# Optimization experiments

Measured on AMD Instinct MI355X. Metric: run time of the kernel, lower is better.

## Reference

```python
import jax, jax.numpy as jnp
import numpy as np

H = 2; C = 64          # heads, hidden_channels
N = 50000; E = 800000  # nodes, edges
D = 128                # input_dim
EPS = 1e-5

def _lrelu(x, s):
    return jnp.where(x >= 0, x, s * x)

def _ln(x, g, b):
    m = x.mean(-1, keepdims=True)
    v = ((x - m) ** 2).mean(-1, keepdims=True)
    return (x - m) / jnp.sqrt(v + EPS) * g + b

def _gatv2(x_src, x_dst, src, dst, Wl, bl, Wr, br, att, Wres, bias):
    # PyG GATv2Conv: concat=False (mean over heads), residual=True, no self loops
    n = x_dst.shape[0]
    xl = (x_src @ Wl + bl).reshape(-1, H, C)  # [Ns,H,C]
    xr = (x_dst @ Wr + br).reshape(-1, H, C)  # [Nd,H,C]
    xj = xl[src]                               # [E,H,C] messages from source
    xi = xr[dst]                               # [E,H,C]
    e = _lrelu(xi + xj, 0.2)
    alpha = jnp.einsum('ehc,hc->eh', e, att)   # [E,H]
    amax = jax.lax.stop_gradient(jax.ops.segment_max(alpha, dst, num_segments=n))
    ex = jnp.exp(alpha - amax[dst])
    den = jax.ops.segment_sum(ex, dst, num_segments=n)
    a = ex / den[dst]                          # segment softmax over incoming edges
    out = jax.ops.segment_sum(xj * a[:, :, None], dst, num_segments=n)  # [Nd,H,C]
    return out.mean(axis=1) + x_dst @ Wres + bias


def setup_inputs() -> dict:
    key = jax.random.key(0)
    ks = jax.random.split(key, 40)
    d = {}
    d['x'] = jax.random.normal(ks[0], (N, D), jnp.float32)
    d['edge_index'] = jax.random.randint(ks[1], (2, E), 0, N, jnp.int32)
    i = 2
    for p, ind in (('c1d', D), ('c1t', D), ('c2d', C), ('c2t', C)):
        d[p + '_Wl'] = jax.random.normal(ks[i], (ind, H * C), jnp.float32) * 0.05; i += 1
        d[p + '_bl'] = jnp.zeros((H * C,), jnp.float32)
        d[p + '_Wr'] = jax.random.normal(ks[i], (ind, H * C), jnp.float32) * 0.05; i += 1
        d[p + '_br'] = jnp.zeros((H * C,), jnp.float32)
        d[p + '_att'] = jax.random.normal(ks[i], (H, C), jnp.float32) * 0.05; i += 1
        d[p + '_Wres'] = jax.random.normal(ks[i], (ind, C), jnp.float32) * 0.05; i += 1
        d[p + '_bias'] = jnp.zeros((C,), jnp.float32)
    d['nd_g'] = jnp.ones((C,), jnp.float32); d['nd_b'] = jnp.zeros((C,), jnp.float32)
    d['nt_g'] = jnp.ones((C,), jnp.float32); d['nt_b'] = jnp.zeros((C,), jnp.float32)
    return d


def reference(x, edge_index, c1d_Wl, c1d_bl, c1d_Wr, c1d_br, c1d_att, c1d_Wres, c1d_bias, c1t_Wl, c1t_bl, c1t_Wr, c1t_br, c1t_att, c1t_Wres, c1t_bias, c2d_Wl, c2d_bl, c2d_Wr, c2d_br, c2d_att, c2d_Wres, c2d_bias, c2t_Wl, c2t_bl, c2t_Wr, c2t_br, c2t_att, c2t_Wres, c2t_bias, nd_g, nd_b, nt_g, nt_b):
    src, dst = edge_index[0], edge_index[1]
    dep = _gatv2(x, x, src, dst, c1d_Wl, c1d_bl, c1d_Wr, c1d_br, c1d_att, c1d_Wres, c1d_bias)
    dep = _lrelu(_ln(dep, nd_g, nd_b), 0.01)
    dant = _gatv2(x, x, dst, src, c1t_Wl, c1t_bl, c1t_Wr, c1t_br, c1t_att, c1t_Wres, c1t_bias)
    dant = _lrelu(_ln(dant, nt_g, nt_b), 0.01)
    dep2 = _lrelu(_gatv2(dep, dep, src, dst, c2d_Wl, c2d_bl, c2d_Wr, c2d_br, c2d_att, c2d_Wres, c2d_bias), 0.01)
    dant2 = _lrelu(_gatv2(dant, dant, dst, src, c2t_Wl, c2t_bl, c2t_Wr, c2t_br, c2t_att, c2t_Wres, c2t_bias), 0.01)
    return jnp.concatenate([dep2, dant2, x], axis=-1)
```

## Files before the change

kernel.cpp:

```cpp
#include <hip/hip_runtime.h>
#include <math.h>

typedef unsigned short ushort_t;
typedef __attribute__((ext_vector_type(8))) short short8x;
typedef __attribute__((ext_vector_type(4))) float f32x4;

#define CSHIFT 9
#define CC 12288
#define EPB 4096
#define ECAP 1024
#define NCMAX 128

__device__ __forceinline__ unsigned f2bf(float f) {
  unsigned u = __float_as_uint(f);
  u += 0x7fff + ((u >> 16) & 1);
  return u >> 16;
}
__device__ __forceinline__ float bf2f(ushort_t u) {
  return __uint_as_float(((unsigned)u) << 16);
}
__device__ __forceinline__ float dpp_red8(float v) {
  v += __int_as_float(__builtin_amdgcn_update_dpp(0, __float_as_int(v), 0xB1, 0xF, 0xF, true));
  v += __int_as_float(__builtin_amdgcn_update_dpp(0, __float_as_int(v), 0x4E, 0xF, 0xF, true));
  v += __int_as_float(__builtin_amdgcn_update_dpp(0, __float_as_int(v), 0x141, 0xF, 0xF, true));
  return v;
}

struct GArgs {
  const float* Wl[2];
  const float* bl[2];
  const float* Wr[2];
  const float* br[2];
  const float* Wres[2];
  const float* bias[2];
};

__device__ __forceinline__ float wval1(const GArgs& ga, int col, int k) {
  int dir = col >= 320 ? 1 : 0;
  int cc = col - dir * 320;
  return cc < 128 ? ga.Wl[dir][k * 128 + cc]
       : cc < 256 ? ga.Wr[dir][k * 128 + (cc - 128)]
                  : ga.Wres[dir][k * 64 + (cc - 256)];
}
__device__ __forceinline__ float bval(const GArgs& ga, int col) {
  int dir = col >= 320 ? 1 : 0;
  int cc = col - dir * 320;
  return cc < 128 ? ga.bl[dir][cc]
       : cc < 256 ? ga.br[dir][cc - 128]
                  : ga.bias[dir][cc - 256];
}


__global__ __launch_bounds__(128) void pack_kernel(GArgs g1, GArgs g2,
                                                   ushort_t* __restrict__ WT1,
                                                   ushort_t* __restrict__ WT2,
                                                   float* __restrict__ bc1,
                                                   float* __restrict__ bc2) {
  int b = blockIdx.x;
  int k = threadIdx.x;
  if (b < 640) {
    WT1[b * 128 + k] = (ushort_t)f2bf(wval1(g1, b, k));
  } else if (b < 1280) {
    int c = b - 640;
    int dir = c >= 320 ? 1 : 0;
    int cc = c - dir * 320;
    float v = 0.f;
    if ((k >> 6) == dir) {
      int k2 = k & 63;
      v = cc < 128 ? g2.Wl[dir][k2 * 128 + cc]
        : cc < 256 ? g2.Wr[dir][k2 * 128 + (cc - 128)]
                   : g2.Wres[dir][k2 * 64 + (cc - 256)];
    }
    WT2[c * 128 + k] = (ushort_t)f2bf(v);
  } else {
    for (int c = k; c < 640; c += 128) {
      bc1[c] = bval(g1, c);
      bc2[c] = bval(g2, c);
    }
  }
}


template <int AF32>
__device__ __forceinline__ void gemm_body(const float* Af, const ushort_t* Ab,
                                          const ushort_t* WT, const float* bc,
                                          ushort_t* Y, int N, int rb, int cb,
                                          ushort_t* lds) {
  const int tid = threadIdx.x;
  const int lane = tid & 63;
  const int w = tid >> 6;
  const int m0 = rb * 64;
  const int cbase = cb * 128 + w * 32;

#pragma unroll
  for (int c = 0; c < 4; ++c) {
    int Lb = (tid + c * 256) * 16;
    int row = Lb >> 8, within = Lb & 255;
    int so = within ^ ((row & 7) << 4);
    int grow = m0 + row;
    if (grow >= N) grow = N - 1;
    if (AF32) {
      const float* src = Af + (size_t)grow * 128 + (so >> 1);
      float4 a = *(const float4*)src;
      float4 b = *(const float4*)(src + 4);
      uint4 o;
      o.x = f2bf(a.x) | (f2bf(a.y) << 16);
      o.y = f2bf(a.z) | (f2bf(a.w) << 16);
      o.z = f2bf(b.x) | (f2bf(b.y) << 16);
      o.w = f2bf(b.z) | (f2bf(b.w) << 16);
      ((uint4*)lds)[tid + c * 256] = o;
    } else {
      ((uint4*)lds)[tid + c * 256] = *(const uint4*)(Ab + (size_t)grow * 128 + (so >> 1));
    }
  }

  short8x bf[4][2];
#pragma unroll
  for (int ks = 0; ks < 4; ++ks)
#pragma unroll
    for (int ns = 0; ns < 2; ++ns) {
      int col = cbase + ns * 16 + (lane & 15);
      bf[ks][ns] = *(const short8x*)(WT + (size_t)col * 128 + ks * 32 + (lane >> 4) * 8);
    }

  __syncthreads();

  f32x4 z = {0.f, 0.f, 0.f, 0.f};
  f32x4 acc[4][2];
#pragma unroll
  for (int ms = 0; ms < 4; ++ms) {
    acc[ms][0] = z;
    acc[ms][1] = z;
  }
#pragma unroll
  for (int ks = 0; ks < 4; ++ks) {
    short8x af[4];
#pragma unroll
    for (int ms = 0; ms < 4; ++ms) {
      int row = ms * 16 + (lane & 15);
      int byte = row * 256 + ((ks * 64 + (lane >> 4) * 16) ^ ((row & 7) << 4));
      af[ms] = *(const short8x*)((const char*)lds + byte);
    }
#pragma unroll
    for (int ms = 0; ms < 4; ++ms) {
      acc[ms][0] = __builtin_amdgcn_mfma_f32_16x16x32_bf16(af[ms], bf[ks][0], acc[ms][0], 0, 0, 0);
      acc[ms][1] = __builtin_amdgcn_mfma_f32_16x16x32_bf16(af[ms], bf[ks][1], acc[ms][1], 0, 0, 0);
    }
  }

#pragma unroll
  for (int ms = 0; ms < 4; ++ms)
#pragma unroll
    for (int ns = 0; ns < 2; ++ns) {
      int col = cbase + ns * 16 + (lane & 15);
      float bv = bc[col];
#pragma unroll
      for (int r = 0; r < 4; ++r) {
        int grow = m0 + ms * 16 + (lane >> 4) * 4 + r;
        if (grow < N) Y[(size_t)grow * 640 + col] = (ushort_t)f2bf(acc[ms][ns][r] + bv);
      }
    }
}


__global__ __launch_bounds__(256) void k_front(
    const float* __restrict__ x, const int* __restrict__ ei, int E, int N,
    int* __restrict__ gc0, int* __restrict__ gc1, int* __restrict__ ctail0,
    int* __restrict__ ctail1, const ushort_t* __restrict__ WT1,
    const float* __restrict__ bc1, ushort_t* __restrict__ Y,
    float* __restrict__ out, int nbinA, int ngemm, int nrow) {
  __shared__ ushort_t lds[8192];
  const int bid = blockIdx.x;
  const int t = threadIdx.x;
  if (bid < nbinA) {
    int* h0 = (int*)lds;
    int* h1 = h0 + NCMAX;
    int* b0 = h1 + NCMAX;
    int* b1 = b0 + NCMAX;
    const int e0 = bid * EPB;
    const int e1 = min(e0 + EPB, E);
    for (int i = t; i < NCMAX; i += 256) {
      h0[i] = 0;
      h1[i] = 0;
    }
    __syncthreads();
    for (int i = e0 + t; i < e1; i += 256) {
      int s = ei[i], d = ei[E + i];
      atomicAdd(&h0[d >> CSHIFT], 1);
      atomicAdd(&h1[s >> CSHIFT], 1);
    }
    __syncthreads();
    for (int c = t; c < NCMAX; c += 256) {
      int n0 = h0[c], n1 = h1[c];
      b0[c] = n0 ? atomicAdd(&ctail0[c], n0) : 0;
      b1[c] = n1 ? atomicAdd(&ctail1[c], n1) : 0;
      h0[c] = 0;
      h1[c] = 0;
    }
    __syncthreads();
    for (int i = e0 + t; i < e1; i += 256) {
      int s = ei[i], d = ei[E + i];
      int c0 = d >> CSHIFT;
      int p0 = b0[c0] + atomicAdd(&h0[c0], 1);
      if (p0 < CC) gc0[c0 * CC + p0] = (s << 16) | d;
      int c1 = s >> CSHIFT;
      int p1 = b1[c1] + atomicAdd(&h1[c1], 1);
      if (p1 < CC) gc1[c1 * CC + p1] = (d << 16) | s;
    }
  } else if (bid < nbinA + ngemm) {
    int gb = bid - nbinA;
    gemm_body<1>(x, nullptr, WT1, bc1, Y, N, gb % nrow, gb / nrow, lds);
  } else {
    int i = (bid - nbinA - ngemm) * 256 + t;
    if (i < N * 32) {
      float4 v = ((const float4*)x)[i];
      ((float4*)out)[(size_t)(i >> 5) * 64 + 32 + (i & 31)] = v;
    }
  }
}


__global__ __launch_bounds__(256) void gemm2_kernel(const ushort_t* __restrict__ A,
                                                    const ushort_t* __restrict__ WT,
                                                    const float* __restrict__ bc,
                                                    ushort_t* __restrict__ Y, int N) {
  __shared__ ushort_t lds[8192];
  gemm_body<0>(nullptr, A, WT, bc, Y, N, blockIdx.x, blockIdx.y, lds);
}


template <int MODE>
__global__ __launch_bounds__(256) void agg_bucket(
    const ushort_t* __restrict__ Y, const int* __restrict__ gc0,
    const int* __restrict__ gc1, const int* __restrict__ ctail0,
    const int* __restrict__ ctail1, const float* __restrict__ attA,
    const float* __restrict__ attB, const float* __restrict__ lng0,
    const float* __restrict__ lnb0, const float* __restrict__ lng1,
    const float* __restrict__ lnb1, void* __restrict__ outp, int N) {
  __shared__ int ebuf[ECAP];
  __shared__ int lnbr[ECAP + 8];
  __shared__ int hist[32], offs[32], cur[32];
  __shared__ int ecnt;
  const int fb = blockIdx.x;
  const int cb = fb >> 4;
  const int dir = blockIdx.y;
  const int t = threadIdx.x;
  const int* gc = dir ? gc1 : gc0;
  const int* ctail = dir ? ctail1 : ctail0;
  const float* att = dir ? attB : attA;

  for (int i = t; i < ECAP + 8; i += 256) lnbr[i] = 0;
  if (t < 32) {
    hist[t] = 0;
    cur[t] = 0;
  }
  if (t == 64) ecnt = 0;
  __syncthreads();

  {
    const int cntc = min(ctail[cb], CC);
    const int* src = gc + cb * CC;
    for (int i = t; i < cntc; i += 256) {
      int e = src[i];
      if (((e & 0xFFFF) >> 5) == fb) {
        int idx = atomicAdd(&ecnt, 1);
        if (idx < ECAP) ebuf[idx] = e;
      }
    }
  }
  __syncthreads();
  const int tot = min(ecnt, ECAP);
  for (int i = t; i < tot; i += 256) atomicAdd(&hist[ebuf[i] & 31], 1);
  __syncthreads();
  if (t < 32) {
    int v = hist[t], inc = v;
#pragma unroll
    for (int o = 1; o < 32; o <<= 1) {
      int u = __shfl_up(inc, o);
      if (t >= o) inc += u;
    }
    offs[t] = inc - v;
  }
  __syncthreads();
  for (int i = t; i < tot; i += 256) {
    int e = ebuf[i];
    int r = e & 31;
    lnbr[offs[r] + atomicAdd(&cur[r], 1)] = (int)((unsigned)e >> 16) * 1280;
  }
  __syncthreads();

  const int wv = t >> 6, lane = t & 63, g = lane >> 4, jj = lane & 15;
  const float L2E = 1.4426950408889634f;
  float av[8];
  {
    float4 a0 = *(const float4*)(att + jj * 8);
    float4 a1 = *(const float4*)(att + jj * 8 + 4);
    av[0] = a0.x * L2E; av[1] = a0.y * L2E; av[2] = a0.z * L2E; av[3] = a0.w * L2E;
    av[4] = a1.x * L2E; av[5] = a1.y * L2E; av[6] = a1.z * L2E; av[7] = a1.w * L2E;
  }
  const char* Yb = (const char*)Y + dir * 640 + jj * 16;

  for (int r = wv; r < 32; r += 4) {
    const int n = fb * 32 + r;
    if (n >= N) break;
    const char* rowp = (const char*)Y + (size_t)n * 1280 + dir * 640;

    float xi[8];
    {
      short8x v = *(const short8x*)(rowp + 256 + jj * 16);
#pragma unroll
      for (int q = 0; q < 8; ++q) xi[q] = bf2f((ushort_t)v[q]);
    }
    float d = 0.f;
    float acc[8];
#pragma unroll
    for (int q = 0; q < 8; ++q) acc[q] = 0.f;

    const int beg = offs[r], deg = hist[r];
    if (deg > 0) {
      int off = lnbr[beg + g];
      short8x vj = *(const short8x*)(Yb + (size_t)(unsigned)off);
      for (int k0 = 0; k0 < deg; k0 += 4) {
        int offn = lnbr[beg + k0 + 4 + g];
        short8x vn = *(const short8x*)(Yb + (size_t)(unsigned)offn);
        float xj[8];
#pragma unroll
        for (int q = 0; q < 8; ++q) xj[q] = bf2f((ushort_t)vj[q]);
        float p = 0.f;
#pragma unroll
        for (int q = 0; q < 8; ++q) {
          float e = xi[q] + xj[q];
          e = fmaxf(e, 0.2f * e);
          p = fmaf(e, av[q], p);
        }
        p = dpp_red8(p);
        float wgt = (k0 + g < deg) ? __builtin_amdgcn_exp2f(p) : 0.f;
        d += wgt;
#pragma unroll
        for (int q = 0; q < 8; ++q) acc[q] = fmaf(xj[q], wgt, acc[q]);
        vj = vn;
      }
#pragma unroll
      for (int o = 16; o <= 32; o <<= 1) {
        d += __shfl_xor(d, o);
#pragma unroll
        for (int q = 0; q < 8; ++q) acc[q] += __shfl_xor(acc[q], o);
      }
    }
    float inv = deg > 0 ? 1.f / d : 0.f;
    float v[8];
#pragma unroll
    for (int q = 0; q < 8; ++q) {
      float tq = acc[q] * inv;
      v[q] = 0.5f * (tq + __shfl_xor(tq, 8));
    }
    {
      short8x rv = *(const short8x*)(rowp + 512 + (jj & 7) * 16);
#pragma unroll
      for (int q = 0; q < 8; ++q) v[q] += bf2f((ushort_t)rv[q]);
    }

    if (MODE == 0) {
      float s = 0.f;
#pragma unroll
      for (int q = 0; q < 8; ++q) s += v[q];
      s += __shfl_xor(s, 1);
      s += __shfl_xor(s, 2);
      s += __shfl_xor(s, 4);
      float mu = s * (1.f / 64.f);
      float vs = 0.f;
#pragma unroll
      for (int q = 0; q < 8; ++q) {
        float dv = v[q] - mu;
        vs += dv * dv;
      }
      vs += __shfl_xor(vs, 1);
      vs += __shfl_xor(vs, 2);
      vs += __shfl_xor(vs, 4);
      float rstd = rsqrtf(vs * (1.f / 64.f) + 1e-5f);
      if (g == 0 && jj < 8) {
        const float* lg = dir ? lng1 : lng0;
        const float* lb = dir ? lnb1 : lnb0;
        unsigned o2[8];
#pragma unroll
        for (int q = 0; q < 8; ++q) {
          int c = jj * 8 + q;
          float y = (v[q] - mu) * rstd * lg[c] + lb[c];
          y = fmaxf(y, 0.01f * y);
          o2[q] = f2bf(y);
        }
        uint4 pk;
        pk.x = o2[0] | (o2[1] << 16);
        pk.y = o2[2] | (o2[3] << 16);
        pk.z = o2[4] | (o2[5] << 16);
        pk.w = o2[6] | (o2[7] << 16);
        *(uint4*)((ushort_t*)outp + (size_t)n * 128 + dir * 64 + jj * 8) = pk;
      }
    } else {
      if (g == 0 && jj < 8) {
        float* op = (float*)outp + (size_t)n * 256 + dir * 64 + jj * 8;
        float4 o0, o1;
        o0.x = fmaxf(v[0], 0.01f * v[0]);
        o0.y = fmaxf(v[1], 0.01f * v[1]);
        o0.z = fmaxf(v[2], 0.01f * v[2]);
        o0.w = fmaxf(v[3], 0.01f * v[3]);
        o1.x = fmaxf(v[4], 0.01f * v[4]);
        o1.y = fmaxf(v[5], 0.01f * v[5]);
        o1.z = fmaxf(v[6], 0.01f * v[6]);
        o1.w = fmaxf(v[7], 0.01f * v[7]);
        *(float4*)op = o0;
        *(float4*)(op + 4) = o1;
      }
    }
  }
}


extern "C" void kernel_launch(void* const* d_in, const int* in_sizes, int n_in,
                              void* d_out, int out_size, void* d_ws, size_t ws_size,
                              hipStream_t stream) {
  const float* x = (const float*)d_in[0];
  const int* ei = (const int*)d_in[1];
  const int N = in_sizes[0] / 128;
  const int E = in_sizes[1] / 2;
  float* out = (float*)d_out;
  const int nbuck = (N + 31) >> 5;
  const int ncoarse = (N + (1 << CSHIFT) - 1) >> CSHIFT;

  char* p = (char*)d_ws;
  auto carve = [&](size_t bytes) {
    char* q = p;
    p += ((bytes + 255) & ~(size_t)255);
    return q;
  };
  int* ctail = (int*)carve(2 * NCMAX * 4);
  int* gc0 = (int*)carve((size_t)ncoarse * CC * 4);
  int* gc1 = (int*)carve((size_t)ncoarse * CC * 4);
  ushort_t* Y1 = (ushort_t*)carve((size_t)N * 640 * 2);
  ushort_t* A2 = (ushort_t*)carve((size_t)N * 128 * 2);
  ushort_t* WT1 = (ushort_t*)carve(640 * 128 * 2);
  ushort_t* WT2 = (ushort_t*)carve(640 * 128 * 2);
  float* bc1 = (float*)carve(640 * 4);
  float* bc2 = (float*)carve(640 * 4);
  int* ctail0 = ctail;
  int* ctail1 = ctail + NCMAX;

  auto F = [&](int i) { return (const float*)d_in[i]; };
  GArgs g1, g2;
  g1.Wl[0] = F(2);  g1.bl[0] = F(3);  g1.Wr[0] = F(4);  g1.br[0] = F(5);
  g1.Wres[0] = F(7); g1.bias[0] = F(8);
  g1.Wl[1] = F(9);  g1.bl[1] = F(10); g1.Wr[1] = F(11); g1.br[1] = F(12);
  g1.Wres[1] = F(14); g1.bias[1] = F(15);
  g2.Wl[0] = F(16); g2.bl[0] = F(17); g2.Wr[0] = F(18); g2.br[0] = F(19);
  g2.Wres[0] = F(21); g2.bias[0] = F(22);
  g2.Wl[1] = F(23); g2.bl[1] = F(24); g2.Wr[1] = F(25); g2.br[1] = F(26);
  g2.Wres[1] = F(28); g2.bias[1] = F(29);

  hipMemsetAsync(ctail, 0, 2 * NCMAX * 4, stream);

  pack_kernel<<<1281, 128, 0, stream>>>(g1, g2, WT1, WT2, bc1, bc2);

  const int nbinA = (E + EPB - 1) / EPB;
  const int nrow = (N + 63) / 64;
  const int ngemm = nrow * 5;
  const int ncopy = (N * 32 + 255) / 256;
  k_front<<<nbinA + ngemm + ncopy, 256, 0, stream>>>(
      x, ei, E, N, gc0, gc1, ctail0, ctail1, WT1, bc1, Y1, out,
      nbinA, ngemm, nrow);

  const dim3 ga(nbuck, 2);
  agg_bucket<0><<<ga, 256, 0, stream>>>(Y1, gc0, gc1, ctail0, ctail1, F(6), F(13),
                                        F(30), F(31), F(32), F(33), A2, N);
  gemm2_kernel<<<dim3(nrow, 5), 256, 0, stream>>>(A2, WT2, bc2, Y1, N);
  agg_bucket<1><<<ga, 256, 0, stream>>>(Y1, gc0, gc1, ctail0, ctail1, F(20), F(27),
                                        nullptr, nullptr, nullptr, nullptr, out, N);
}
```

Measured before the change: 305.8 us.

## Split LeakyReLU attention into abs term plus precomputed per-source exponential factor

Rewrites LeakyReLU(e) as 0.6e + 0.4|e|. The destination-only linear term cancels in the softmax, and the source-only linear term becomes a per-node factor exp(0.6·att·(W_l x + b_l)), computed by new kmat blocks in the front and second-layer GEMM kernels and stored in bf16. The per-edge inner loop then needs only an fabs-weighted dot product and one multiply by the gathered factor, instead of a max and an extra multiply per channel. In exchange it adds an extra 2-byte gather per edge, new precompute blocks, and some bf16 rounding of the exponential factor.

```diff
diff --git a/kernel.cpp b/kernel.cpp
--- a/kernel.cpp
+++ b/kernel.cpp
@@ -11,6 +11,9 @@
 #define ECAP 1024
 #define NCMAX 128
 
+#define C06L2E 0.8656170245333781f
+#define C04L2E 0.5770780163555854f
+
 __device__ __forceinline__ unsigned f2bf(float f) {
   unsigned u = __float_as_uint(f);
   u += 0x7fff + ((u >> 16) & 1);
@@ -23,6 +26,11 @@
   v += __int_as_float(__builtin_amdgcn_update_dpp(0, __float_as_int(v), 0xB1, 0xF, 0xF, true));
   v += __int_as_float(__builtin_amdgcn_update_dpp(0, __float_as_int(v), 0x4E, 0xF, 0xF, true));
   v += __int_as_float(__builtin_amdgcn_update_dpp(0, __float_as_int(v), 0x141, 0xF, 0xF, true));
+  return v;
+}
+__device__ __forceinline__ float dpp_red16(float v) {
+  v = dpp_red8(v);
+  v += __int_as_float(__builtin_amdgcn_update_dpp(0, __float_as_int(v), 0x140, 0xF, 0xF, true));
   return v;
 }
 
@@ -51,11 +59,13 @@
 }
 
 
-__global__ __launch_bounds__(128) void pack_kernel(GArgs g1, GArgs g2,
-                                                   ushort_t* __restrict__ WT1,
-                                                   ushort_t* __restrict__ WT2,
-                                                   float* __restrict__ bc1,
-                                                   float* __restrict__ bc2) {
+__global__ __launch_bounds__(128) void pack_kernel(
+    GArgs g1, GArgs g2, const float* __restrict__ a1d0,
+    const float* __restrict__ a1d1, const float* __restrict__ a2d0,
+    const float* __restrict__ a2d1, ushort_t* __restrict__ WT1,
+    ushort_t* __restrict__ WT2, float* __restrict__ bc1,
+    float* __restrict__ bc2, float* __restrict__ WS1,
+    float* __restrict__ WS2, float* __restrict__ sb) {
   int b = blockIdx.x;
   int k = threadIdx.x;
   if (b < 640) {
@@ -72,10 +82,37 @@
                    : g2.Wres[dir][k2 * 64 + (cc - 256)];
     }
     WT2[c * 128 + k] = (ushort_t)f2bf(v);
-  } else {
+  } else if (b == 1280) {
     for (int c = k; c < 640; c += 128) {
       bc1[c] = bval(g1, c);
       bc2[c] = bval(g2, c);
+    }
+  } else {
+    const float* att1[2] = {a1d0, a1d1};
+    const float* att2[2] = {a2d0, a2d1};
+#pragma unroll
+    for (int t = 0; t < 4; ++t) {
+      int dir = t >> 1, h = t & 1;
+      float s1 = 0.f;
+      for (int c = 0; c < 64; ++c)
+        s1 += att1[dir][h * 64 + c] * g1.Wl[dir][k * 128 + h * 64 + c];
+      WS1[k * 4 + t] = s1;
+      float s2 = 0.f;
+      if ((k >> 6) == dir) {
+        int k2 = k & 63;
+        for (int c = 0; c < 64; ++c)
+          s2 += att2[dir][h * 64 + c] * g2.Wl[dir][k2 * 128 + h * 64 + c];
+      }
+      WS2[k * 4 + t] = s2;
+    }
+    if (k < 8) {
+      int t = k & 3;
+      int dir = t >> 1, h = t & 1;
+      const float* att = (k < 4) ? (dir ? a1d1 : a1d0) : (dir ? a2d1 : a2d0);
+      const float* bl = (k < 4) ? g1.bl[dir] : g2.bl[dir];
+      float s = 0.f;
+      for (int c = 0; c < 64; ++c) s += att[h * 64 + c] * bl[h * 64 + c];
+      sb[k] = s;
     }
   }
 }
@@ -163,12 +200,65 @@
 }
 
 
+template <int AF32>
+__device__ __forceinline__ void kmat_body(const float* Af, const ushort_t* Ab,
+                                          const float* __restrict__ WS,
+                                          const float* __restrict__ sbp,
+                                          ushort_t* __restrict__ K, int kb, int N) {
+  const int t = threadIdx.x;
+  const int jj = t & 15;
+  float wsr[8][4];
+#pragma unroll
+  for (int q = 0; q < 8; ++q) {
+    float4 w = *(const float4*)(WS + (jj * 8 + q) * 4);
+    wsr[q][0] = w.x; wsr[q][1] = w.y; wsr[q][2] = w.z; wsr[q][3] = w.w;
+  }
+  float sb4[4] = {sbp[0], sbp[1], sbp[2], sbp[3]};
+#pragma unroll
+  for (int it = 0; it < 4; ++it) {
+    int n = kb * 64 + it * 16 + (t >> 4);
+    if (n >= N) continue;
+    float xv[8];
+    if (AF32) {
+      const float* src = Af + (size_t)n * 128 + jj * 8;
+      float4 a = *(const float4*)src;
+      float4 b = *(const float4*)(src + 4);
+      xv[0] = a.x; xv[1] = a.y; xv[2] = a.z; xv[3] = a.w;
+      xv[4] = b.x; xv[5] = b.y; xv[6] = b.z; xv[7] = b.w;
+    } else {
+      short8x v = *(const short8x*)(Ab + (size_t)n * 128 + jj * 8);
+#pragma unroll
+      for (int q = 0; q < 8; ++q) xv[q] = bf2f((ushort_t)v[q]);
+    }
+    float s[4] = {0.f, 0.f, 0.f, 0.f};
+#pragma unroll
+    for (int q = 0; q < 8; ++q)
+#pragma unroll
+      for (int t4 = 0; t4 < 4; ++t4) s[t4] = fmaf(xv[q], wsr[q][t4], s[t4]);
+#pragma unroll
+    for (int t4 = 0; t4 < 4; ++t4) s[t4] = dpp_red16(s[t4]);
+    if (jj == 0) {
+      unsigned kk[4];
+#pragma unroll
+      for (int t4 = 0; t4 < 4; ++t4)
+        kk[t4] = f2bf(__builtin_amdgcn_exp2f(C06L2E * (s[t4] + sb4[t4])));
+      uint2 pk;
+      pk.x = kk[0] | (kk[1] << 16);
+      pk.y = kk[2] | (kk[3] << 16);
+      *(uint2*)(K + (size_t)n * 4) = pk;
+    }
+  }
+}
+
+
 __global__ __launch_bounds__(256) void k_front(
     const float* __restrict__ x, const int* __restrict__ ei, int E, int N,
     int* __restrict__ gc0, int* __restrict__ gc1, int* __restrict__ ctail0,
     int* __restrict__ ctail1, const ushort_t* __restrict__ WT1,
-    const float* __restrict__ bc1, ushort_t* __restrict__ Y,
-    float* __restrict__ out, int nbinA, int ngemm, int nrow) {
+    const float* __restrict__ bc1, const float* __restrict__ WS1,
+    const float* __restrict__ sb, ushort_t* __restrict__ K1,
+    ushort_t* __restrict__ Y, float* __restrict__ out, int nbinA, int ngemm,
+    int nrow, int ncopy) {
   __shared__ ushort_t lds[8192];
   const int bid = blockIdx.x;
   const int t = threadIdx.x;
@@ -210,12 +300,14 @@
   } else if (bid < nbinA + ngemm) {
     int gb = bid - nbinA;
     gemm_body<1>(x, nullptr, WT1, bc1, Y, N, gb % nrow, gb / nrow, lds);
-  } else {
+  } else if (bid < nbinA + ngemm + ncopy) {
     int i = (bid - nbinA - ngemm) * 256 + t;
     if (i < N * 32) {
       float4 v = ((const float4*)x)[i];
       ((float4*)out)[(size_t)(i >> 5) * 64 + 32 + (i & 31)] = v;
     }
+  } else {
+    kmat_body<1>(x, nullptr, WS1, sb, K1, bid - nbinA - ngemm - ncopy, N);
   }
 }
 
@@ -223,9 +315,16 @@
 __global__ __launch_bounds__(256) void gemm2_kernel(const ushort_t* __restrict__ A,
                                                     const ushort_t* __restrict__ WT,
                                                     const float* __restrict__ bc,
+                                                    const float* __restrict__ WS2,
+                                                    const float* __restrict__ sb,
+                                                    ushort_t* __restrict__ K2,
                                                     ushort_t* __restrict__ Y, int N) {
   __shared__ ushort_t lds[8192];
-  gemm_body<0>(nullptr, A, WT, bc, Y, N, blockIdx.x, blockIdx.y, lds);
+  if (blockIdx.y < 5) {
+    gemm_body<0>(nullptr, A, WT, bc, Y, N, blockIdx.x, blockIdx.y, lds);
+  } else {
+    kmat_body<0>(nullptr, A, WS2, sb + 4, K2, blockIdx.x, N);
+  }
 }
 
 
@@ -233,10 +332,11 @@
 __global__ __launch_bounds__(256) void agg_bucket(
     const ushort_t* __restrict__ Y, const int* __restrict__ gc0,
     const int* __restrict__ gc1, const int* __restrict__ ctail0,
-    const int* __restrict__ ctail1, const float* __restrict__ attA,
-    const float* __restrict__ attB, const float* __restrict__ lng0,
-    const float* __restrict__ lnb0, const float* __restrict__ lng1,
-    const float* __restrict__ lnb1, void* __restrict__ outp, int N) {
+    const int* __restrict__ ctail1, const ushort_t* __restrict__ Kv,
+    const float* __restrict__ attA, const float* __restrict__ attB,
+    const float* __restrict__ lng0, const float* __restrict__ lnb0,
+    const float* __restrict__ lng1, const float* __restrict__ lnb1,
+    void* __restrict__ outp, int N) {
   __shared__ int ebuf[ECAP];
   __shared__ int lnbr[ECAP + 8];
   __shared__ int hist[32], offs[32], cur[32];
@@ -285,20 +385,20 @@
   for (int i = t; i < tot; i += 256) {
     int e = ebuf[i];
     int r = e & 31;
-    lnbr[offs[r] + atomicAdd(&cur[r], 1)] = (int)((unsigned)e >> 16) * 1280;
+    lnbr[offs[r] + atomicAdd(&cur[r], 1)] = (int)((unsigned)e >> 16);
   }
   __syncthreads();
 
   const int wv = t >> 6, lane = t & 63, g = lane >> 4, jj = lane & 15;
-  const float L2E = 1.4426950408889634f;
   float av[8];
   {
     float4 a0 = *(const float4*)(att + jj * 8);
     float4 a1 = *(const float4*)(att + jj * 8 + 4);
-    av[0] = a0.x * L2E; av[1] = a0.y * L2E; av[2] = a0.z * L2E; av[3] = a0.w * L2E;
-    av[4] = a1.x * L2E; av[5] = a1.y * L2E; av[6] = a1.z * L2E; av[7] = a1.w * L2E;
+    av[0] = a0.x * C04L2E; av[1] = a0.y * C04L2E; av[2] = a0.z * C04L2E; av[3] = a0.w * C04L2E;
+    av[4] = a1.x * C04L2E; av[5] = a1.y * C04L2E; av[6] = a1.z * C04L2E; av[7] = a1.w * C04L2E;
   }
   const char* Yb = (const char*)Y + dir * 640 + jj * 16;
+  const int koff = dir * 2 + (jj >> 3);
 
   for (int r = wv; r < 32; r += 4) {
     const int n = fb * 32 + r;
@@ -318,11 +418,13 @@
 
     const int beg = offs[r], deg = hist[r];
     if (deg > 0) {
-      int off = lnbr[beg + g];
-      short8x vj = *(const short8x*)(Yb + (size_t)(unsigned)off);
+      int jc = lnbr[beg + g];
+      short8x vj = *(const short8x*)(Yb + (size_t)(unsigned)(jc * 1280));
+      float Kc = bf2f(Kv[jc * 4 + koff]);
       for (int k0 = 0; k0 < deg; k0 += 4) {
-        int offn = lnbr[beg + k0 + 4 + g];
-        short8x vn = *(const short8x*)(Yb + (size_t)(unsigned)offn);
+        int jn = lnbr[beg + k0 + 4 + g];
+        short8x vn = *(const short8x*)(Yb + (size_t)(unsigned)(jn * 1280));
+        float Kn = bf2f(Kv[jn * 4 + koff]);
         float xj[8];
 #pragma unroll
         for (int q = 0; q < 8; ++q) xj[q] = bf2f((ushort_t)vj[q]);
@@ -330,15 +432,15 @@
 #pragma unroll
         for (int q = 0; q < 8; ++q) {
           float e = xi[q] + xj[q];
-          e = fmaxf(e, 0.2f * e);
-          p = fmaf(e, av[q], p);
+          p = fmaf(av[q], __builtin_fabsf(e), p);
         }
         p = dpp_red8(p);
-        float wgt = (k0 + g < deg) ? __builtin_amdgcn_exp2f(p) : 0.f;
+        float wgt = (k0 + g < deg) ? __builtin_amdgcn_exp2f(p) * Kc : 0.f;
         d += wgt;
 #pragma unroll
         for (int q = 0; q < 8; ++q) acc[q] = fmaf(xj[q], wgt, acc[q]);
         vj = vn;
+        Kc = Kn;
       }
 #pragma unroll
       for (int o = 16; o <= 32; o <<= 1) {
@@ -442,6 +544,11 @@
   ushort_t* WT2 = (ushort_t*)carve(640 * 128 * 2);
   float* bc1 = (float*)carve(640 * 4);
   float* bc2 = (float*)carve(640 * 4);
+  float* WS1 = (float*)carve(128 * 4 * 4);
+  float* WS2 = (float*)carve(128 * 4 * 4);
+  float* sb = (float*)carve(8 * 4);
+  ushort_t* K1 = (ushort_t*)carve((size_t)N * 4 * 2);
+  ushort_t* K2 = (ushort_t*)carve((size_t)N * 4 * 2);
   int* ctail0 = ctail;
   int* ctail1 = ctail + NCMAX;
 
@@ -458,20 +565,23 @@
 
   hipMemsetAsync(ctail, 0, 2 * NCMAX * 4, stream);
 
-  pack_kernel<<<1281, 128, 0, stream>>>(g1, g2, WT1, WT2, bc1, bc2);
+  pack_kernel<<<1282, 128, 0, stream>>>(g1, g2, F(6), F(13), F(20), F(27),
+                                        WT1, WT2, bc1, bc2, WS1, WS2, sb);
 
   const int nbinA = (E + EPB - 1) / EPB;
   const int nrow = (N + 63) / 64;
   const int ngemm = nrow * 5;
   const int ncopy = (N * 32 + 255) / 256;
-  k_front<<<nbinA + ngemm + ncopy, 256, 0, stream>>>(
-      x, ei, E, N, gc0, gc1, ctail0, ctail1, WT1, bc1, Y1, out,
-      nbinA, ngemm, nrow);
+  k_front<<<nbinA + ngemm + ncopy + nrow, 256, 0, stream>>>(
+      x, ei, E, N, gc0, gc1, ctail0, ctail1, WT1, bc1, WS1, sb, K1, Y1, out,
+      nbinA, ngemm, nrow, ncopy);
 
   const dim3 ga(nbuck, 2);
-  agg_bucket<0><<<ga, 256, 0, stream>>>(Y1, gc0, gc1, ctail0, ctail1, F(6), F(13),
-                                        F(30), F(31), F(32), F(33), A2, N);
-  gemm2_kernel<<<dim3(nrow, 5), 256, 0, stream>>>(A2, WT2, bc2, Y1, N);
-  agg_bucket<1><<<ga, 256, 0, stream>>>(Y1, gc0, gc1, ctail0, ctail1, F(20), F(27),
-                                        nullptr, nullptr, nullptr, nullptr, out, N);
-}
+  agg_bucket<0><<<ga, 256, 0, stream>>>(Y1, gc0, gc1, ctail0, ctail1, K1,
+                                        F(6), F(13), F(30), F(31), F(32), F(33),
+                                        A2, N);
+  gemm2_kernel<<<dim3(nrow, 6), 256, 0, stream>>>(A2, WT2, bc2, WS2, sb, K2, Y1, N);
+  agg_bucket<1><<<ga, 256, 0, stream>>>(Y1, gc0, gc1, ctail0, ctail1, K2,
+                                        F(20), F(27), nullptr, nullptr, nullptr,
+                                        nullptr, out, N);
+}
```

Measured after the change: 327.2 us. 7.0% more time.
